# Performance work log

Hardware: AMD Instinct MI355X
Metric: run time of the kernel (lower is better)

Reference implementation:

```python
import jax, jax.numpy as jnp
import numpy as np

KS = 3            # kernel_size
DILS = (1, 2, 4)  # dilation_list == padding_list
EPS = 1e-5        # BN eps


def _unfold3(x, d):
    # emulate F.unfold(kernel=3, dilation=d, padding=d, stride=1).view(b, c, 9, h, w)
    b, c, h, w = x.shape
    xp = jnp.pad(x, ((0, 0), (0, 0), (d, d), (d, d)))
    pats = [xp[:, :, i * d:i * d + h, j * d:j * d + w] for i in range(KS) for j in range(KS)]
    return jnp.stack(pats, axis=2)


def _conv1x1(x, w, b):
    return jnp.einsum('bchw,oc->bohw', x, w) + b[None, :, None, None]


def _bn_relu(x, g, be, m, v):
    s = g / jnp.sqrt(v + EPS)
    return jax.nn.relu(x * s[None, :, None, None] + (be - m * s)[None, :, None, None])


def _proj(x, w1, b1, g1, be1, m1, v1, w2, b2, g2, be2, m2, v2):
    h = _bn_relu(_conv1x1(x, w1, b1), g1, be1, m1, v1)
    return _bn_relu(_conv1x1(h, w2, b2), g2, be2, m2, v2)


def setup_inputs():
    key = jax.random.key(0)
    Cin, Ck, Cv, Cout = 512, 256, 256, 512
    B, H, W = 4, 64, 64
    ks = iter(jax.random.split(key, 48))

    def nrm(shape, s=0.02):
        return jax.random.normal(next(ks), shape, jnp.float32) * s

    def bn(c):
        return (jnp.ones((c,), jnp.float32) + nrm((c,), 0.1),  # gamma
                nrm((c,), 0.1),                                 # beta
                nrm((c,), 0.1),                                 # running mean
                jax.random.uniform(next(ks), (c,), jnp.float32, 0.5, 1.5))  # running var

    inp = {"x": jax.random.normal(next(ks), (B, Cin, H, W), jnp.float32)}
    for p in ("k", "q"):
        g1, be1, m1, v1 = bn(Ck)
        g2, be2, m2, v2 = bn(Ck)
        inp.update({
            p + "1_w": nrm((Ck, Cin)), p + "1_b": nrm((Ck,)),
            p + "1_g": g1, p + "1_be": be1, p + "1_m": m1, p + "1_v": v1,
            p + "2_w": nrm((Ck, Ck)), p + "2_b": nrm((Ck,)),
            p + "2_g": g2, p + "2_be": be2, p + "2_m": m2, p + "2_v": v2,
        })
    inp["v_w"] = nrm((Cv, Cin)); inp["v_b"] = nrm((Cv,))
    inp["w_w"] = nrm((Cout, Cv)); inp["w_b"] = nrm((Cout,))
    return inp


def reference(x,
              k1_w, k1_b, k1_g, k1_be, k1_m, k1_v,
              k2_w, k2_b, k2_g, k2_be, k2_m, k2_v,
              q1_w, q1_b, q1_g, q1_be, q1_m, q1_v,
              q2_w, q2_b, q2_g, q2_be, q2_m, q2_v,
              v_w, v_b, w_w, w_b):
    # scale == 1: MaxPool2d(1x1-equivalent) and final bilinear resize are identities.
    value = _conv1x1(x, v_w, v_b)                                  # (b,cv,h,w)
    keyf = _proj(x, k1_w, k1_b, k1_g, k1_be, k1_m, k1_v,
                 k2_w, k2_b, k2_g, k2_be, k2_m, k2_v)              # (b,ck,h,w)
    query = _proj(x, q1_w, q1_b, q1_g, q1_be, q1_m, q1_v,
                  q2_w, q2_b, q2_g, q2_be, q2_m, q2_v)             # (b,ck,h,w)
    uk = jnp.concatenate([_unfold3(keyf, d) for d in DILS], axis=2)   # (b,ck,27,h,w)
    uv = jnp.concatenate([_unfold3(value, d) for d in DILS], axis=2)  # (b,cv,27,h,w)
    sim = jnp.sum(uk * query[:, :, None], axis=1, keepdims=True)      # (b,1,27,h,w)
    sim = jax.nn.softmax(sim, axis=2)
    context = jnp.sum(sim * uv, axis=2)                               # (b,cv,h,w)
    return _conv1x1(context, w_w, w_b)
```

## Files before the change

### kernel.cpp

```cpp
#include <hip/hip_runtime.h>

#define HW   4096
#define Hh   64
#define Ww   64
#define NB   27
#define EPSBN 1e-5f

typedef _Float16 f16x8 __attribute__((ext_vector_type(8)));
typedef _Float16 f16x4 __attribute__((ext_vector_type(4)));
typedef _Float16 f16x2 __attribute__((ext_vector_type(2)));
typedef float    f32x4 __attribute__((ext_vector_type(4)));

__device__ __forceinline__ void gld_lds16(const void* g, void* l) {
    __builtin_amdgcn_global_load_lds(
        (const __attribute__((address_space(1))) unsigned int*)g,
        (__attribute__((address_space(3))) unsigned int*)l, 16, 0, 0);
}

__global__ __launch_bounds__(256)
void prep_kernel(const float* s0, const float* s1, const float* s2,
                 const float* s3, const float* s4, const float* s5,
                 _Float16* d0, _Float16* d1, _Float16* d2,
                 _Float16* d3, _Float16* d4, _Float16* d5,
                 const float* __restrict__ x, _Float16* __restrict__ xT)
{
    __shared__ _Float16 T[64][516];
    const int bid = blockIdx.x;
    const int tid = threadIdx.x;

    if (bid < 384) {
        const int j  = bid >> 6;
        const int bx = bid & 63;
        const float* s = j==0?s0: j==1?s1: j==2?s2: j==3?s3: j==4?s4: s5;
        _Float16*  d = j==0?d0: j==1?d1: j==2?d2: j==3?d3: j==4?d4: d5;
        const int  n = (j==3 || j==4) ? 65536 : 131072;
        const int  i = (bx * 256 + tid) * 8;
        if (i < n) {
            f16x8 h;
            #pragma unroll
            for (int k = 0; k < 8; ++k) h[k] = (_Float16)s[i + k];
            *(f16x8*)(d + i) = h;
        }
        return;
    }
    const int t  = bid - 384;
    const int p0 = (t & 63) * 64;
    const int b  = t >> 6;
    const int tx = tid & 63;
    const int ty = tid >> 6;

    #pragma unroll 2
    for (int ch = 0; ch < 16; ++ch) {
        const int c0 = ch * 32 + ty * 8;
        const float* xp = x + ((size_t)b * 512 + c0) * HW + p0 + tx;
        f16x8 h;
        #pragma unroll
        for (int i = 0; i < 8; ++i) h[i] = (_Float16)xp[(size_t)i * HW];
        *(f16x8*)&T[tx][c0] = h;
    }
    __syncthreads();
    #pragma unroll 4
    for (int rr = 0; rr < 16; ++rr) {
        const int row = rr * 4 + ty;
        f16x8 h = *(const f16x8*)&T[row][tx * 8];
        *(f16x8*)(xT + ((size_t)b * HW + p0 + row) * 512 + tx * 8) = h;
    }
}

struct GJob {
    const _Float16* in;
    const _Float16* w;
    const float* b; const float* g; const float* be; const float* m; const float* v;
    _Float16* oh;
    float*    of;
};

__global__ __launch_bounds__(256)
void gemm128(GJob J0, GJob J1, GJob J2, int nmb0, int nmb01,
             int K, int JO, int mode)
{
    __shared__ _Float16 As[2][128 * 64];
    __shared__ _Float16 Bs[2][128 * 64];

    const int tid  = threadIdx.x;
    const int lane = tid & 63;
    const int w    = tid >> 6;
    const int lr   = lane & 15;
    const int lg   = lane >> 4;
    const int wm   = w & 1;
    const int wn   = w >> 1;

    const int bx = blockIdx.x;
    const int nb = (bx & 7) * 16 + (bx >> 3);
    const int mb = blockIdx.y;

    const bool i0 = mb < nmb0;
    const bool i1 = !i0 && mb < nmb01;
#define SELJ(f) (i0 ? J0.f : (i1 ? J1.f : J2.f))
    const _Float16* Jin = SELJ(in);
    const _Float16* Jw  = SELJ(w);
    const float* Jb  = SELJ(b);
    const float* Jg  = SELJ(g);
    const float* Jbe = SELJ(be);
    const float* Jm  = SELJ(m);
    const float* Jv  = SELJ(v);
    _Float16* Joh = SELJ(oh);
    float*    Jof = SELJ(of);
#undef SELJ
    const int obase = (mb - (i0 ? 0 : (i1 ? nmb0 : nmb01))) * 128;

    const int rowS = w * 32 + (lane >> 3);
    const int scol = (((lane & 7) ^ (lane >> 3)) << 3);
    const _Float16* aSrc = Jw  + (size_t)(obase + rowS) * K + scol;
    const _Float16* bSrc = Jin + (size_t)(nb * 128 + rowS) * K + scol;

    auto STAGE = [&](int buf, int rd) {
        const int kb = rd * 64;
        char* aD = (char*)&As[buf][0] + w * 4096;
        char* bD = (char*)&Bs[buf][0] + w * 4096;
        #pragma unroll
        for (int j = 0; j < 4; ++j)
            gld_lds16(aSrc + (size_t)j * 8 * K + kb, aD + j * 1024);
        #pragma unroll
        for (int j = 0; j < 4; ++j)
            gld_lds16(bSrc + (size_t)j * 8 * K + kb, bD + j * 1024);
    };

    f32x4 acc[4][4] = {};

    const int nr = K >> 6;
    STAGE(0, 0);
    __syncthreads();

    int cur = 0;
    for (int rd = 0; rd < nr; ++rd) {
        if (rd + 1 < nr) STAGE(cur ^ 1, rd + 1);
        #pragma unroll
        for (int ks = 0; ks < 2; ++ks) {
            const int colx = (ks * 64 + lg * 16) ^ ((lr & 7) << 4);
            f16x8 afr[4], bfr[4];
            #pragma unroll
            for (int t = 0; t < 4; ++t) {
                afr[t] = *(const f16x8*)((const char*)&As[cur][0] + (wm * 64 + t * 16 + lr) * 128 + colx);
                bfr[t] = *(const f16x8*)((const char*)&Bs[cur][0] + (wn * 64 + t * 16 + lr) * 128 + colx);
            }
            #pragma unroll
            for (int ai = 0; ai < 4; ++ai)
                #pragma unroll
                for (int bj = 0; bj < 4; ++bj)
                    acc[ai][bj] = __builtin_amdgcn_mfma_f32_16x16x32_f16(
                        afr[ai], bfr[bj], acc[ai][bj], 0, 0, 0);
        }
        __syncthreads();
        cur ^= 1;
    }

    const int relu = (Jg != nullptr);
    #pragma unroll
    for (int ai = 0; ai < 4; ++ai) {
        const int o4 = obase + wm * 64 + ai * 16 + lg * 4;
        float sc[4], of_[4];
        #pragma unroll
        for (int r = 0; r < 4; ++r) {
            const int o = o4 + r;
            if (Jg) { float s = Jg[o] * rsqrtf(Jv[o] + EPSBN); sc[r] = s; of_[r] = fmaf(Jb[o] - Jm[o], s, Jbe[o]); }
            else    { sc[r] = 1.f; of_[r] = Jb[o]; }
        }
        #pragma unroll
        for (int bj = 0; bj < 4; ++bj) {
            const int pg = nb * 128 + wn * 64 + bj * 16 + lr;
            float vv[4];
            #pragma unroll
            for (int r = 0; r < 4; ++r) {
                float t = fmaf(acc[ai][bj][r], sc[r], of_[r]);
                vv[r] = relu ? fmaxf(t, 0.f) : t;
            }
            if (mode == 0) {
                f16x4 h;
                #pragma unroll
                for (int r = 0; r < 4; ++r) h[r] = (_Float16)vv[r];
                *(f16x4*)(Joh + (size_t)pg * JO + o4) = h;
            } else {
                #pragma unroll
                for (int r = 0; r < 4; ++r)
                    Jof[((size_t)(pg >> 12) * JO + o4 + r) * HW + (pg & 4095)] = vv[r];
            }
        }
    }
}

__global__ __launch_bounds__(256)
void attn_fused(const _Float16* __restrict__ keyT, const _Float16* __restrict__ qryT,
                const _Float16* __restrict__ valT, _Float16* __restrict__ ctxT)
{
    const int tid  = threadIdx.x;
    const int slot = tid & 31;
    const int b    = blockIdx.y;
    const int p    = blockIdx.x * 8 + (tid >> 5);
    const int y    = p >> 6;
    const int xc   = p & 63;

    int   idx[NB];
    float valf[NB];
    #pragma unroll
    for (int n = 0; n < NB; ++n) {
        const int d  = (n < 9) ? 1 : (n < 18 ? 2 : 4);
        const int i  = (n / 3) % 3 - 1;
        const int j  = n % 3 - 1;
        const int yy = y + i * d, xx = xc + j * d;
        const bool ok = ((unsigned)yy < (unsigned)Hh) && ((unsigned)xx < (unsigned)Ww);
        idx[n]  = min(max(yy, 0), Hh - 1) * Ww + min(max(xx, 0), Ww - 1);
        valf[n] = ok ? 1.f : 0.f;
    }

    const size_t base = (size_t)b * HW * 256 + slot * 8;
    const f16x8 q8 = *(const f16x8*)(qryT + base + (size_t)p * 256);

    f16x2 qp[4];
    qp[0] = __builtin_shufflevector(q8, q8, 0, 1);
    qp[1] = __builtin_shufflevector(q8, q8, 2, 3);
    qp[2] = __builtin_shufflevector(q8, q8, 4, 5);
    qp[3] = __builtin_shufflevector(q8, q8, 6, 7);

    float sim[NB];
    #pragma unroll
    for (int n = 0; n < NB; ++n) {
        const f16x8 k8 = *(const f16x8*)(keyT + base + (size_t)idx[n] * 256);
        float s = 0.f;
        s = __builtin_amdgcn_fdot2(__builtin_shufflevector(k8, k8, 0, 1), qp[0], s, false);
        s = __builtin_amdgcn_fdot2(__builtin_shufflevector(k8, k8, 2, 3), qp[1], s, false);
        s = __builtin_amdgcn_fdot2(__builtin_shufflevector(k8, k8, 4, 5), qp[2], s, false);
        s = __builtin_amdgcn_fdot2(__builtin_shufflevector(k8, k8, 6, 7), qp[3], s, false);
        sim[n] = s;
    }

    #pragma unroll
    for (int n = 0; n < NB; ++n) {
        float s = sim[n];
        s += __shfl_xor(s, 1);
        s += __shfl_xor(s, 2);
        s += __shfl_xor(s, 4);
        s += __shfl_xor(s, 8);
        s += __shfl_xor(s, 16);
        sim[n] = s * valf[n];
    }

    float mx = sim[0];
    #pragma unroll
    for (int n = 1; n < NB; ++n) mx = fmaxf(mx, sim[n]);
    float sum = 0.f;
    #pragma unroll
    for (int n = 0; n < NB; ++n) { sim[n] = __expf(sim[n] - mx); sum += sim[n]; }
    const float inv = 1.f / sum;
    #pragma unroll
    for (int n = 0; n < NB; ++n) sim[n] = sim[n] * inv * valf[n];

    float acc[8];
    #pragma unroll
    for (int i = 0; i < 8; ++i) acc[i] = 0.f;
    #pragma unroll
    for (int n = 0; n < NB; ++n) {
        const f16x8 v8 = *(const f16x8*)(valT + base + (size_t)idx[n] * 256);
        const float w = sim[n];
        #pragma unroll
        for (int i = 0; i < 8; ++i) acc[i] = fmaf(w, (float)v8[i], acc[i]);
    }

    f16x8 h;
    #pragma unroll
    for (int i = 0; i < 8; ++i) h[i] = (_Float16)acc[i];
    *(f16x8*)(ctxT + base + (size_t)p * 256) = h;
}

extern "C" void kernel_launch(void* const* d_in, const int* in_sizes, int n_in,
                              void* d_out, int out_size, void* d_ws, size_t ws_size,
                              hipStream_t stream)
{
    (void)in_sizes; (void)n_in; (void)out_size; (void)ws_size;
    const float* x     = (const float*)d_in[0];
    const float* k1_w  = (const float*)d_in[1];
    const float* k1_b  = (const float*)d_in[2];
    const float* k1_g  = (const float*)d_in[3];
    const float* k1_be = (const float*)d_in[4];
    const float* k1_m  = (const float*)d_in[5];
    const float* k1_v  = (const float*)d_in[6];
    const float* k2_w  = (const float*)d_in[7];
    const float* k2_b  = (const float*)d_in[8];
    const float* k2_g  = (const float*)d_in[9];
    const float* k2_be = (const float*)d_in[10];
    const float* k2_m  = (const float*)d_in[11];
    const float* k2_v  = (const float*)d_in[12];
    const float* q1_w  = (const float*)d_in[13];
    const float* q1_b  = (const float*)d_in[14];
    const float* q1_g  = (const float*)d_in[15];
    const float* q1_be = (const float*)d_in[16];
    const float* q1_m  = (const float*)d_in[17];
    const float* q1_v  = (const float*)d_in[18];
    const float* q2_w  = (const float*)d_in[19];
    const float* q2_b  = (const float*)d_in[20];
    const float* q2_g  = (const float*)d_in[21];
    const float* q2_be = (const float*)d_in[22];
    const float* q2_m  = (const float*)d_in[23];
    const float* q2_v  = (const float*)d_in[24];
    const float* v_w   = (const float*)d_in[25];
    const float* v_b   = (const float*)d_in[26];
    const float* w_w   = (const float*)d_in[27];
    const float* w_b   = (const float*)d_in[28];

    _Float16* hw = (_Float16*)d_ws;
    const size_t SX = (size_t)4 * HW * 512;
    const size_t SH = (size_t)4 * HW * 256;
    _Float16* xT    = hw;
    _Float16* wv_h  = xT + SX;
    _Float16* wk1_h = wv_h  + 131072;
    _Float16* wq1_h = wk1_h + 131072;
    _Float16* wk2_h = wq1_h + 131072;
    _Float16* wq2_h = wk2_h + 65536;
    _Float16* ww_h  = wq2_h + 65536;
    _Float16* k1T   = ww_h  + 131072;
    _Float16* q1T   = k1T + SH;
    _Float16* valT  = q1T + SH;
    _Float16* ctxT  = valT + SH;
    _Float16* keyPC = ctxT + SH;
    _Float16* qryPC = keyPC + SH;

    prep_kernel<<<640, 256, 0, stream>>>(v_w, k1_w, q1_w, k2_w, q2_w, w_w,
                                         wv_h, wk1_h, wq1_h, wk2_h, wq2_h, ww_h,
                                         x, xT);

    GJob jv  = { xT,  wv_h,  v_b,  nullptr, nullptr, nullptr, nullptr, valT,  nullptr };
    GJob jk1 = { xT,  wk1_h, k1_b, k1_g, k1_be, k1_m, k1_v,            k1T,   nullptr };
    GJob jq1 = { xT,  wq1_h, q1_b, q1_g, q1_be, q1_m, q1_v,            q1T,   nullptr };
    GJob jk2 = { k1T, wk2_h, k2_b, k2_g, k2_be, k2_m, k2_v,            keyPC, nullptr };
    GJob jq2 = { q1T, wq2_h, q2_b, q2_g, q2_be, q2_m, q2_v,            qryPC, nullptr };
    GJob jw  = { ctxT, ww_h, w_b,  nullptr, nullptr, nullptr, nullptr, nullptr, (float*)d_out };

    gemm128<<<dim3(128, 6), 256, 0, stream>>>(jv, jk1, jq1, 2, 4, 512, 256, 0);
    gemm128<<<dim3(128, 4), 256, 0, stream>>>(jk2, jq2, jq2, 2, 4, 256, 256, 0);
    attn_fused<<<dim3(512, 4), 256, 0, stream>>>(keyPC, qryPC, valT, ctxT);
    gemm128<<<dim3(128, 4), 256, 0, stream>>>(jw, jw, jw, 4, 4, 256, 512, 2);
}
```

Baseline: 98.35 us.

## Fuse x fp32-to-fp16 transpose into first GEMM's B-tile staging

Removes the separate x transpose/convert pass in the prep kernel. The first GEMM now loads fp32 x directly from NCHW into registers, converts it to fp16 and writes it swizzled into LDS, with the next tile's loads overlapped against the MFMA work. This avoids writing and re-reading a 16 MB fp16 copy of x. In exchange, each M-block re-reads fp32 x from global memory, which is six times across the fused v/k1/q1 GEMM, and register pressure rises. The grid is also flattened to 1D so that blocks sharing an N tile are grouped on the same XCD, which should improve L2 reuse of x.

```diff
diff --git a/kernel.cpp b/kernel.cpp
--- a/kernel.cpp
+++ b/kernel.cpp
@@ -21,54 +21,26 @@
 void prep_kernel(const float* s0, const float* s1, const float* s2,
                  const float* s3, const float* s4, const float* s5,
                  _Float16* d0, _Float16* d1, _Float16* d2,
-                 _Float16* d3, _Float16* d4, _Float16* d5,
-                 const float* __restrict__ x, _Float16* __restrict__ xT)
+                 _Float16* d3, _Float16* d4, _Float16* d5)
 {
-    __shared__ _Float16 T[64][516];
     const int bid = blockIdx.x;
-    const int tid = threadIdx.x;
-
-    if (bid < 384) {
-        const int j  = bid >> 6;
-        const int bx = bid & 63;
-        const float* s = j==0?s0: j==1?s1: j==2?s2: j==3?s3: j==4?s4: s5;
-        _Float16*  d = j==0?d0: j==1?d1: j==2?d2: j==3?d3: j==4?d4: d5;
-        const int  n = (j==3 || j==4) ? 65536 : 131072;
-        const int  i = (bx * 256 + tid) * 8;
-        if (i < n) {
-            f16x8 h;
-            #pragma unroll
-            for (int k = 0; k < 8; ++k) h[k] = (_Float16)s[i + k];
-            *(f16x8*)(d + i) = h;
-        }
-        return;
-    }
-    const int t  = bid - 384;
-    const int p0 = (t & 63) * 64;
-    const int b  = t >> 6;
-    const int tx = tid & 63;
-    const int ty = tid >> 6;
-
-    #pragma unroll 2
-    for (int ch = 0; ch < 16; ++ch) {
-        const int c0 = ch * 32 + ty * 8;
-        const float* xp = x + ((size_t)b * 512 + c0) * HW + p0 + tx;
+    const int j  = bid >> 6;
+    const int bx = bid & 63;
+    const float* s = j==0?s0: j==1?s1: j==2?s2: j==3?s3: j==4?s4: s5;
+    _Float16*  d = j==0?d0: j==1?d1: j==2?d2: j==3?d3: j==4?d4: d5;
+    const int  n = (j==3 || j==4) ? 65536 : 131072;
+    const int  i = (bx * 256 + threadIdx.x) * 8;
+    if (i < n) {
         f16x8 h;
         #pragma unroll
-        for (int i = 0; i < 8; ++i) h[i] = (_Float16)xp[(size_t)i * HW];
-        *(f16x8*)&T[tx][c0] = h;
-    }
-    __syncthreads();
-    #pragma unroll 4
-    for (int rr = 0; rr < 16; ++rr) {
-        const int row = rr * 4 + ty;
-        f16x8 h = *(const f16x8*)&T[row][tx * 8];
-        *(f16x8*)(xT + ((size_t)b * HW + p0 + row) * 512 + tx * 8) = h;
+        for (int k = 0; k < 8; ++k) h[k] = (_Float16)s[i + k];
+        *(f16x8*)(d + i) = h;
     }
 }
 
 struct GJob {
     const _Float16* in;
+    const float*    xf;
     const _Float16* w;
     const float* b; const float* g; const float* be; const float* m; const float* v;
     _Float16* oh;
@@ -76,7 +48,7 @@
 };
 
 __global__ __launch_bounds__(256)
-void gemm128(GJob J0, GJob J1, GJob J2, int nmb0, int nmb01,
+void gemm128(GJob J0, GJob J1, GJob J2, int nmb0, int nmb01, int nmbTot,
              int K, int JO, int mode)
 {
     __shared__ _Float16 As[2][128 * 64];
@@ -90,14 +62,17 @@
     const int wm   = w & 1;
     const int wn   = w >> 1;
 
-    const int bx = blockIdx.x;
-    const int nb = (bx & 7) * 16 + (bx >> 3);
-    const int mb = blockIdx.y;
+    const int bid = blockIdx.x;
+    const int xcd = bid & 7;
+    const int jj  = bid >> 3;
+    const int nb  = xcd * 16 + jj / nmbTot;
+    const int mb  = jj % nmbTot;
 
     const bool i0 = mb < nmb0;
     const bool i1 = !i0 && mb < nmb01;
 #define SELJ(f) (i0 ? J0.f : (i1 ? J1.f : J2.f))
     const _Float16* Jin = SELJ(in);
+    const float*    Jxf = SELJ(xf);
     const _Float16* Jw  = SELJ(w);
     const float* Jb  = SELJ(b);
     const float* Jg  = SELJ(g);
@@ -111,30 +86,70 @@
 
     const int rowS = w * 32 + (lane >> 3);
     const int scol = (((lane & 7) ^ (lane >> 3)) << 3);
-    const _Float16* aSrc = Jw  + (size_t)(obase + rowS) * K + scol;
-    const _Float16* bSrc = Jin + (size_t)(nb * 128 + rowS) * K + scol;
-
-    auto STAGE = [&](int buf, int rd) {
+    const _Float16* aSrc = Jw + (size_t)(obase + rowS) * K + scol;
+    const _Float16* bSrc = Jin ? (Jin + (size_t)(nb * 128 + rowS) * K + scol) : nullptr;
+
+    const int h    = w & 1;
+    const int q    = w >> 1;
+    const int brow = h * 64 + lane;
+    const int bxor = (brow & 7) << 4;
+    const float* xbase = nullptr;
+    if (Jxf) {
+        const int bb = nb >> 5;
+        const int pp = (nb & 31) * 128 + h * 64 + lane;
+        xbase = Jxf + (size_t)bb * 512 * HW + pp;
+    }
+
+    float fr[4][8];
+
+    auto STAGE_A = [&](int buf, int rd) {
         const int kb = rd * 64;
         char* aD = (char*)&As[buf][0] + w * 4096;
+        #pragma unroll
+        for (int j2 = 0; j2 < 4; ++j2)
+            gld_lds16(aSrc + (size_t)j2 * 8 * K + kb, aD + j2 * 1024);
+    };
+    auto STAGE_B_LDS = [&](int buf, int rd) {
+        const int kb = rd * 64;
         char* bD = (char*)&Bs[buf][0] + w * 4096;
         #pragma unroll
-        for (int j = 0; j < 4; ++j)
-            gld_lds16(aSrc + (size_t)j * 8 * K + kb, aD + j * 1024);
-        #pragma unroll
-        for (int j = 0; j < 4; ++j)
-            gld_lds16(bSrc + (size_t)j * 8 * K + kb, bD + j * 1024);
+        for (int j2 = 0; j2 < 4; ++j2)
+            gld_lds16(bSrc + (size_t)j2 * 8 * K + kb, bD + j2 * 1024);
     };
+    auto ISSUE_BX = [&](int rd) {
+        const int kb = rd * 64 + q * 32;
+        #pragma unroll
+        for (int g2 = 0; g2 < 4; ++g2)
+            #pragma unroll
+            for (int i2 = 0; i2 < 8; ++i2)
+                fr[g2][i2] = xbase[(size_t)(kb + g2 * 8 + i2) * HW];
+    };
+    auto WRITE_BX = [&](int buf) {
+        #pragma unroll
+        for (int g2 = 0; g2 < 4; ++g2) {
+            f16x8 hv;
+            #pragma unroll
+            for (int i2 = 0; i2 < 8; ++i2) hv[i2] = (_Float16)fr[g2][i2];
+            *(f16x8*)((char*)&Bs[buf][0] + brow * 128 + ((q * 64 + g2 * 16) ^ bxor)) = hv;
+        }
+    };
 
     f32x4 acc[4][4] = {};
-
     const int nr = K >> 6;
-    STAGE(0, 0);
+
+    if (Jxf) { ISSUE_BX(0); WRITE_BX(0); }
+    else     { STAGE_B_LDS(0, 0); }
+    STAGE_A(0, 0);
     __syncthreads();
 
     int cur = 0;
     for (int rd = 0; rd < nr; ++rd) {
-        if (rd + 1 < nr) STAGE(cur ^ 1, rd + 1);
+        const bool more = (rd + 1 < nr);
+        if (more) {
+            STAGE_A(cur ^ 1, rd + 1);
+            if (Jxf) ISSUE_BX(rd + 1);
+            else     STAGE_B_LDS(cur ^ 1, rd + 1);
+        }
         #pragma unroll
         for (int ks = 0; ks < 2; ++ks) {
             const int colx = (ks * 64 + lg * 16) ^ ((lr & 7) << 4);
@@ -151,6 +166,7 @@
                     acc[ai][bj] = __builtin_amdgcn_mfma_f32_16x16x32_f16(
                         afr[ai], bfr[bj], acc[ai][bj], 0, 0, 0);
         }
+        if (Jxf && more) WRITE_BX(cur ^ 1);
         __syncthreads();
         cur ^= 1;
     }
@@ -176,10 +192,10 @@
                 vv[r] = relu ? fmaxf(t, 0.f) : t;
             }
             if (mode == 0) {
-                f16x4 h;
+                f16x4 hh;
                 #pragma unroll
-                for (int r = 0; r < 4; ++r) h[r] = (_Float16)vv[r];
-                *(f16x4*)(Joh + (size_t)pg * JO + o4) = h;
+                for (int r = 0; r < 4; ++r) hh[r] = (_Float16)vv[r];
+                *(f16x4*)(Joh + (size_t)pg * JO + o4) = hh;
             } else {
                 #pragma unroll
                 for (int r = 0; r < 4; ++r)
@@ -308,10 +324,8 @@
     const float* w_b   = (const float*)d_in[28];
 
     _Float16* hw = (_Float16*)d_ws;
-    const size_t SX = (size_t)4 * HW * 512;
     const size_t SH = (size_t)4 * HW * 256;
-    _Float16* xT    = hw;
-    _Float16* wv_h  = xT + SX;
+    _Float16* wv_h  = hw;
     _Float16* wk1_h = wv_h  + 131072;
     _Float16* wq1_h = wk1_h + 131072;
     _Float16* wk2_h = wq1_h + 131072;
@@ -324,19 +338,18 @@
     _Float16* keyPC = ctxT + SH;
     _Float16* qryPC = keyPC + SH;
 
-    prep_kernel<<<640, 256, 0, stream>>>(v_w, k1_w, q1_w, k2_w, q2_w, w_w,
-                                         wv_h, wk1_h, wq1_h, wk2_h, wq2_h, ww_h,
-                                         x, xT);
-
-    GJob jv  = { xT,  wv_h,  v_b,  nullptr, nullptr, nullptr, nullptr, valT,  nullptr };
-    GJob jk1 = { xT,  wk1_h, k1_b, k1_g, k1_be, k1_m, k1_v,            k1T,   nullptr };
-    GJob jq1 = { xT,  wq1_h, q1_b, q1_g, q1_be, q1_m, q1_v,            q1T,   nullptr };
-    GJob jk2 = { k1T, wk2_h, k2_b, k2_g, k2_be, k2_m, k2_v,            keyPC, nullptr };
-    GJob jq2 = { q1T, wq2_h, q2_b, q2_g, q2_be, q2_m, q2_v,            qryPC, nullptr };
-    GJob jw  = { ctxT, ww_h, w_b,  nullptr, nullptr, nullptr, nullptr, nullptr, (float*)d_out };
-
-    gemm128<<<dim3(128, 6), 256, 0, stream>>>(jv, jk1, jq1, 2, 4, 512, 256, 0);
-    gemm128<<<dim3(128, 4), 256, 0, stream>>>(jk2, jq2, jq2, 2, 4, 256, 256, 0);
+    prep_kernel<<<384, 256, 0, stream>>>(v_w, k1_w, q1_w, k2_w, q2_w, w_w,
+                                         wv_h, wk1_h, wq1_h, wk2_h, wq2_h, ww_h);
+
+    GJob jv  = { nullptr, x, wv_h,  v_b,  nullptr, nullptr, nullptr, nullptr, valT,  nullptr };
+    GJob jk1 = { nullptr, x, wk1_h, k1_b, k1_g, k1_be, k1_m, k1_v,            k1T,   nullptr };
+    GJob jq1 = { nullptr, x, wq1_h, q1_b, q1_g, q1_be, q1_m, q1_v,            q1T,   nullptr };
+    GJob jk2 = { k1T, nullptr, wk2_h, k2_b, k2_g, k2_be, k2_m, k2_v,          keyPC, nullptr };
+    GJob jq2 = { q1T, nullptr, wq2_h, q2_b, q2_g, q2_be, q2_m, q2_v,          qryPC, nullptr };
+    GJob jw  = { ctxT, nullptr, ww_h, w_b,  nullptr, nullptr, nullptr, nullptr, nullptr, (float*)d_out };
+
+    gemm128<<<768, 256, 0, stream>>>(jv, jk1, jq1, 2, 4, 6, 512, 256, 0);
+    gemm128<<<512, 256, 0, stream>>>(jk2, jq2, jq2, 2, 4, 4, 256, 256, 0);
     attn_fused<<<dim3(512, 4), 256, 0, stream>>>(keyPC, qryPC, valT, ctxT);
-    gemm128<<<dim3(128, 4), 256, 0, stream>>>(jw, jw, jw, 4, 4, 256, 512, 2);
-}
+    gemm128<<<512, 256, 0, stream>>>(jw, jw, jw, 4, 4, 4, 256, 512, 2);
+}
```

After: 96.13 us. 1.02x faster.
